# Performance work log

Hardware: AMD Instinct MI355X
Metric: run time of the kernel (lower is better)

## Reference

```python
import jax, jax.numpy as jnp
import numpy as np

N_NODES = 100000
N_EDGES = 1600000
D_IN = 128
D_HID = 128
SCALE = 1.8
EPS = 1e-12


def setup_inputs() -> dict:
    key = jax.random.key(0)
    ks = jax.random.split(key, 7)
    x = jax.random.normal(ks[0], (N_NODES, D_IN), dtype=jnp.float32)
    W1 = jax.random.normal(ks[1], (D_HID, D_IN), dtype=jnp.float32) * 0.05
    b1 = jax.random.normal(ks[2], (D_HID,), dtype=jnp.float32) * 0.05
    W2 = jax.random.normal(ks[3], (D_HID, D_HID), dtype=jnp.float32) * 0.05
    b2 = jax.random.normal(ks[4], (D_HID,), dtype=jnp.float32) * 0.05
    src = jax.random.randint(ks[5], (N_EDGES,), 0, N_NODES, dtype=jnp.int64 if jax.config.jax_enable_x64 else jnp.int32)
    dst = jax.random.randint(ks[6], (N_EDGES,), 0, N_NODES, dtype=jnp.int64 if jax.config.jax_enable_x64 else jnp.int32)
    return {"x": x, "W1": W1, "b1": b1, "W2": W2, "b2": b2, "src": src, "dst": dst}


def reference(x, W1, b1, W2, b2, src, dst):
    N = x.shape[0]
    ones = jnp.ones((src.shape[0],), dtype=x.dtype)
    # GraphConv norm='both' degree normalizers (clamped to >=1 as in DGL)
    deg_out = jnp.maximum(jnp.zeros((N,), x.dtype).at[src].add(ones), 1.0)
    deg_in = jnp.maximum(jnp.zeros((N,), x.dtype).at[dst].add(ones), 1.0)
    norm_out = jax.lax.rsqrt(deg_out)[:, None]  # [N,1]
    norm_in = jax.lax.rsqrt(deg_in)[:, None]    # [N,1]

    def layer(h, W, b):
        # torch.nn.Linear: h @ W.T + b
        h = jnp.einsum('nd,kd->nk', h, W) + b
        # F.normalize(h, dim=1) * 1.8
        nrm = jnp.sqrt(jnp.sum(h * h, axis=1, keepdims=True))
        h = h / jnp.maximum(nrm, EPS) * SCALE
        # GraphConv (weight=False, bias=False, norm='both'):
        # D_out^{-1/2} -> sparse aggregate -> D_in^{-1/2}
        h = h * norm_out
        agg = jax.ops.segment_sum(h[src], dst, num_segments=N)
        return agg * norm_in

    h = layer(x, W1, b1)
    h = layer(h, W2, b2)
    return h
```

## Files before the change

### kernel.cpp

```cpp
#include <hip/hip_runtime.h>
#include <cstdint>
#include <cstddef>

#define D 128
#define NSCALE 1.8f
#define NEPS 1e-12f
#define EPB 8192
#define NLO 512

typedef __attribute__((ext_vector_type(8))) short bf16x8;
typedef __attribute__((ext_vector_type(4))) float f32x4;

__device__ __forceinline__ ushort bf16_rtn(float f) {
    uint32_t u = __float_as_uint(f);
    u = u + 0x7FFFu + ((u >> 16) & 1u);
    return (ushort)(u >> 16);
}

__device__ __forceinline__ float bf16_to_f(ushort u) {
    return __uint_as_float((uint32_t)u << 16);
}

__global__ __launch_bounds__(256) void hist_high_kernel(const int* __restrict__ src,
                                                        const int* __restrict__ dst,
                                                        int* __restrict__ Hd,
                                                        int* __restrict__ Hs, int ne) {
    __shared__ int hd[256], hs[256];
    int t = threadIdx.x, b = blockIdx.x;
    hd[t] = 0; hs[t] = 0;
    __syncthreads();
    int base = b * EPB, end = min(ne, base + EPB);
    for (int i = base + t; i < end; i += 256) {
        atomicAdd(&hd[dst[i] >> 9], 1);
        atomicAdd(&hs[src[i] >> 9], 1);
    }
    __syncthreads();
    Hd[b * 256 + t] = hd[t];
    Hs[b * 256 + t] = hs[t];
}

__global__ __launch_bounds__(256) void scan_cols_kernel(int* __restrict__ Hd,
                                                        int* __restrict__ Hs,
                                                        int* __restrict__ total_d,
                                                        int* __restrict__ total_s, int nbk) {
    __shared__ int s[256];
    int* H = blockIdx.y ? Hs : Hd;
    int* tot = blockIdx.y ? total_s : total_d;
    int v = blockIdx.x, t = threadIdx.x;
    int val = (t < nbk) ? H[t * 256 + v] : 0;
    s[t] = val;
    __syncthreads();
    #pragma unroll
    for (int off = 1; off < 256; off <<= 1) {
        int u = (t >= off) ? s[t - off] : 0;
        __syncthreads();
        s[t] += u;
        __syncthreads();
    }
    if (t < nbk) H[t * 256 + v] = s[t] - val;
    if (t == nbk - 1) tot[v] = s[t];
}

__global__ __launch_bounds__(256) void scan_tot_kernel(const int* __restrict__ total_d,
                                                       const int* __restrict__ total_s,
                                                       int* __restrict__ Bd,
                                                       int* __restrict__ Bs, int hb) {
    __shared__ int s[256];
    const int* tot = blockIdx.x ? total_s : total_d;
    int* B = blockIdx.x ? Bs : Bd;
    int t = threadIdx.x;
    int val = (t < hb) ? tot[t] : 0;
    s[t] = val;
    __syncthreads();
    #pragma unroll
    for (int off = 1; off < 256; off <<= 1) {
        int u = (t >= off) ? s[t - off] : 0;
        __syncthreads();
        s[t] += u;
        __syncthreads();
    }
    if (t <= hb) B[t] = s[t] - val;
}

__global__ __launch_bounds__(256) void scatter_high_kernel(const int* __restrict__ src,
                                                           const int* __restrict__ dst,
                                                           const int* __restrict__ Hd,
                                                           const int* __restrict__ Hs,
                                                           const int* __restrict__ Bd,
                                                           const int* __restrict__ Bs,
                                                           int* __restrict__ sd_dst,
                                                           int* __restrict__ sd_src,
                                                           int* __restrict__ ss_src,
                                                           int ne, int hb) {
    __shared__ int cur_d[256], cur_s[256];
    int t = threadIdx.x, b = blockIdx.x;
    if (t < hb) {
        cur_d[t] = Bd[t] + Hd[b * 256 + t];
        cur_s[t] = Bs[t] + Hs[b * 256 + t];
    }
    __syncthreads();
    int base = b * EPB, end = min(ne, base + EPB);
    for (int i = base + t; i < end; i += 256) {
        int d = dst[i], s = src[i];
        int pd = atomicAdd(&cur_d[d >> 9], 1);
        sd_dst[pd] = d;
        sd_src[pd] = s;
        int ps = atomicAdd(&cur_s[s >> 9], 1);
        ss_src[ps] = s;
    }
}

__global__ __launch_bounds__(512) void bucket_sort_kernel(const int* __restrict__ sd_dst,
                                                          const int* __restrict__ sd_src,
                                                          const int* __restrict__ Bd,
                                                          int* __restrict__ offs,
                                                          int* __restrict__ cnt_dst,
                                                          float* __restrict__ norm_in,
                                                          int* __restrict__ ssrc, int N) {
    __shared__ int h[NLO], sc[NLO], cur[NLO];
    int t = threadIdx.x, v = blockIdx.x;
    int beg = Bd[v], end = Bd[v + 1];
    h[t] = 0;
    __syncthreads();
    for (int i = beg + t; i < end; i += 512) atomicAdd(&h[sd_dst[i] & (NLO - 1)], 1);
    __syncthreads();
    int cnt = h[t];
    sc[t] = cnt;
    __syncthreads();
    #pragma unroll
    for (int off = 1; off < NLO; off <<= 1) {
        int u = (t >= off) ? sc[t - off] : 0;
        __syncthreads();
        sc[t] += u;
        __syncthreads();
    }
    int excl = sc[t] - cnt;
    int g = (v << 9) + t;
    if (g < N) {
        offs[g] = beg + excl;
        cnt_dst[g] = cnt;
        norm_in[g] = rsqrtf((float)max(cnt, 1));
    }
    cur[t] = beg + excl;
    __syncthreads();
    for (int i = beg + t; i < end; i += 512) {
        int d = sd_dst[i];
        int s = sd_src[i];
        int p = atomicAdd(&cur[d & (NLO - 1)], 1);
        ssrc[p] = s;
    }
}

__global__ __launch_bounds__(512) void bucket_hist_kernel(const int* __restrict__ ss_src,
                                                          const int* __restrict__ Bs,
                                                          float* __restrict__ norm_out, int N) {
    __shared__ int h[NLO];
    int t = threadIdx.x, v = blockIdx.x;
    int beg = Bs[v], end = Bs[v + 1];
    h[t] = 0;
    __syncthreads();
    for (int i = beg + t; i < end; i += 512) atomicAdd(&h[ss_src[i] & (NLO - 1)], 1);
    __syncthreads();
    int g = (v << 9) + t;
    if (g < N) norm_out[g] = rsqrtf((float)max(h[t], 1));
}

__global__ __launch_bounds__(256) void mlp_mfma_kernel(const float* __restrict__ X,
                                                       const float* __restrict__ W,
                                                       const float* __restrict__ b,
                                                       const float* __restrict__ post,
                                                       ushort* __restrict__ Abuf, int N) {
    __shared__ ushort Wf[128 * 128];

    const int t = threadIdx.x;
    const int wave = t >> 6;
    const int lane = t & 63;
    const int q = lane >> 4;
    const int l16 = lane & 15;

    #pragma unroll
    for (int it = 0; it < 8; ++it) {
        int f = t + 256 * it;
        int j = f >> 8;
        int p = (f >> 6) & 3;
        int ln = f & 63;
        int n = 16 * j + (ln & 15);
        int k0 = 32 * p + 8 * (ln >> 4);
        const float* srcp = W + n * D + k0;
        float4 a0 = *(const float4*)(srcp);
        float4 a1 = *(const float4*)(srcp + 4);
        bf16x8 v;
        v[0] = (short)bf16_rtn(a0.x); v[1] = (short)bf16_rtn(a0.y);
        v[2] = (short)bf16_rtn(a0.z); v[3] = (short)bf16_rtn(a0.w);
        v[4] = (short)bf16_rtn(a1.x); v[5] = (short)bf16_rtn(a1.y);
        v[6] = (short)bf16_rtn(a1.z); v[7] = (short)bf16_rtn(a1.w);
        ((bf16x8*)Wf)[f] = v;
    }

    const int r0 = blockIdx.x * 128 + wave * 32;
    bf16x8 ahi[2][4], alo[2][4];
    #pragma unroll
    for (int rt = 0; rt < 2; ++rt) {
        int row = r0 + rt * 16 + l16;
        bool ok = (row < N);
        const float* xr = X + (size_t)(ok ? row : 0) * D;
        #pragma unroll
        for (int p = 0; p < 4; ++p) {
            int k0 = 32 * p + 8 * q;
            float4 a0 = ok ? *(const float4*)(xr + k0)     : make_float4(0, 0, 0, 0);
            float4 a1 = ok ? *(const float4*)(xr + k0 + 4) : make_float4(0, 0, 0, 0);
            float fv[8] = {a0.x, a0.y, a0.z, a0.w, a1.x, a1.y, a1.z, a1.w};
            bf16x8 h, l;
            #pragma unroll
            for (int e = 0; e < 8; ++e) {
                uint32_t u = __float_as_uint(fv[e]);
                h[e] = (short)(u >> 16);
                float hf = __uint_as_float(u & 0xFFFF0000u);
                l[e] = (short)(__float_as_uint(fv[e] - hf) >> 16);
            }
            ahi[rt][p] = h;
            alo[rt][p] = l;
        }
    }

    __syncthreads();

    f32x4 acc[2][8];
    #pragma unroll
    for (int rt = 0; rt < 2; ++rt)
        #pragma unroll
        for (int j = 0; j < 8; ++j) acc[rt][j] = (f32x4){0.f, 0.f, 0.f, 0.f};

    #pragma unroll
    for (int j = 0; j < 8; ++j) {
        #pragma unroll
        for (int p = 0; p < 4; ++p) {
            bf16x8 bb = ((bf16x8*)Wf)[(j * 4 + p) * 64 + lane];
            acc[0][j] = __builtin_amdgcn_mfma_f32_16x16x32_bf16(ahi[0][p], bb, acc[0][j], 0, 0, 0);
            acc[0][j] = __builtin_amdgcn_mfma_f32_16x16x32_bf16(alo[0][p], bb, acc[0][j], 0, 0, 0);
            acc[1][j] = __builtin_amdgcn_mfma_f32_16x16x32_bf16(ahi[1][p], bb, acc[1][j], 0, 0, 0);
            acc[1][j] = __builtin_amdgcn_mfma_f32_16x16x32_bf16(alo[1][p], bb, acc[1][j], 0, 0, 0);
        }
    }

    float bias[8];
    #pragma unroll
    for (int j = 0; j < 8; ++j) bias[j] = b[16 * j + l16];

    #pragma unroll
    for (int rt = 0; rt < 2; ++rt) {
        float ss[4] = {0.f, 0.f, 0.f, 0.f};
        #pragma unroll
        for (int j = 0; j < 8; ++j)
            #pragma unroll
            for (int r = 0; r < 4; ++r) {
                float v = acc[rt][j][r] + bias[j];
                acc[rt][j][r] = v;
                ss[r] += v * v;
            }
        #pragma unroll
        for (int m = 1; m <= 8; m <<= 1)
            #pragma unroll
            for (int r = 0; r < 4; ++r) ss[r] += __shfl_xor(ss[r], m);

        #pragma unroll
        for (int r = 0; r < 4; ++r) {
            int row = r0 + rt * 16 + 4 * q + r;
            if (row < N) {
                float f = NSCALE / fmaxf(sqrtf(ss[r]), NEPS) * post[row];
                #pragma unroll
                for (int j = 0; j < 8; ++j)
                    Abuf[(size_t)row * D + 16 * j + l16] = bf16_rtn(acc[rt][j][r] * f);
            }
        }
    }
}

__global__ __launch_bounds__(256) void agg_kernel(const ushort* __restrict__ A,
                                                  const int* __restrict__ sorted_src,
                                                  const int* __restrict__ offs,
                                                  const int* __restrict__ cnt,
                                                  const float* __restrict__ norm_in,
                                                  float* __restrict__ out, int N) {
    int g = (blockIdx.x * blockDim.x + threadIdx.x) >> 5;
    int lane = threadIdx.x & 31;
    if (g >= N) return;
    int beg = offs[g];
    int len = cnt[g];
    float4 acc = make_float4(0.f, 0.f, 0.f, 0.f);
    int i = 0;
    for (; i + 4 <= len; i += 4) {
        int s0 = sorted_src[beg + i];
        int s1 = sorted_src[beg + i + 1];
        int s2 = sorted_src[beg + i + 2];
        int s3 = sorted_src[beg + i + 3];
        ushort4 v0 = *(const ushort4*)(A + (size_t)s0 * D + lane * 4);
        ushort4 v1 = *(const ushort4*)(A + (size_t)s1 * D + lane * 4);
        ushort4 v2 = *(const ushort4*)(A + (size_t)s2 * D + lane * 4);
        ushort4 v3 = *(const ushort4*)(A + (size_t)s3 * D + lane * 4);
        acc.x += bf16_to_f(v0.x) + bf16_to_f(v1.x) + bf16_to_f(v2.x) + bf16_to_f(v3.x);
        acc.y += bf16_to_f(v0.y) + bf16_to_f(v1.y) + bf16_to_f(v2.y) + bf16_to_f(v3.y);
        acc.z += bf16_to_f(v0.z) + bf16_to_f(v1.z) + bf16_to_f(v2.z) + bf16_to_f(v3.z);
        acc.w += bf16_to_f(v0.w) + bf16_to_f(v1.w) + bf16_to_f(v2.w) + bf16_to_f(v3.w);
    }
    for (; i < len; ++i) {
        int s = sorted_src[beg + i];
        ushort4 v = *(const ushort4*)(A + (size_t)s * D + lane * 4);
        acc.x += bf16_to_f(v.x);
        acc.y += bf16_to_f(v.y);
        acc.z += bf16_to_f(v.z);
        acc.w += bf16_to_f(v.w);
    }
    float sc = norm_in[g];
    acc.x *= sc; acc.y *= sc; acc.z *= sc; acc.w *= sc;
    *(float4*)(out + (size_t)g * D + lane * 4) = acc;
}


extern "C" void kernel_launch(void* const* d_in, const int* in_sizes, int n_in,
                              void* d_out, int out_size, void* d_ws, size_t ws_size,
                              hipStream_t stream) {
    const float* x  = (const float*)d_in[0];
    const float* W1 = (const float*)d_in[1];
    const float* b1 = (const float*)d_in[2];
    const float* W2 = (const float*)d_in[3];
    const float* b2 = (const float*)d_in[4];
    const int* src  = (const int*)d_in[5];
    const int* dst  = (const int*)d_in[6];
    float* out = (float*)d_out;

    const int N  = in_sizes[0] / D;
    const int NE = in_sizes[5];
    const int NBK = (NE + EPB - 1) / EPB;
    const int HB  = (N + NLO - 1) / NLO;

    char* w = (char*)d_ws;
    auto take = [&](size_t bytes) { char* p = w; w += (bytes + 255) & ~(size_t)255; return p; };
    int*    Hd       = (int*)take((size_t)NBK * 256 * 4);
    int*    Hs       = (int*)take((size_t)NBK * 256 * 4);
    int*    total_d  = (int*)take(256 * 4);
    int*    total_s  = (int*)take(256 * 4);
    int*    Bd       = (int*)take((size_t)(HB + 1) * 4);
    int*    Bs       = (int*)take((size_t)(HB + 1) * 4);
    int*    sd_dst   = (int*)take((size_t)NE * 4);
    int*    sd_src   = (int*)take((size_t)NE * 4);
    int*    ss_src   = (int*)take((size_t)NE * 4);
    int*    ssrc     = (int*)take((size_t)NE * 4);
    int*    offs     = (int*)take((size_t)N * 4);
    int*    cnt_dst  = (int*)take((size_t)N * 4);
    float*  norm_in  = (float*)take((size_t)N * 4);
    float*  norm_out = (float*)take((size_t)N * 4);
    ushort* Abuf     = (ushort*)take((size_t)N * D * 2);

    hist_high_kernel<<<NBK, 256, 0, stream>>>(src, dst, Hd, Hs, NE);
    scan_cols_kernel<<<dim3(HB, 2), 256, 0, stream>>>(Hd, Hs, total_d, total_s, NBK);
    scan_tot_kernel<<<2, 256, 0, stream>>>(total_d, total_s, Bd, Bs, HB);
    scatter_high_kernel<<<NBK, 256, 0, stream>>>(src, dst, Hd, Hs, Bd, Bs,
                                                 sd_dst, sd_src, ss_src, NE, HB);
    bucket_sort_kernel<<<HB, 512, 0, stream>>>(sd_dst, sd_src, Bd, offs, cnt_dst,
                                               norm_in, ssrc, N);
    bucket_hist_kernel<<<HB, 512, 0, stream>>>(ss_src, Bs, norm_out, N);

    const int mlp_blocks = (N + 127) / 128;
    const int agg_blocks = (N * 32 + 255) / 256;

    mlp_mfma_kernel<<<mlp_blocks, 256, 0, stream>>>(x, W1, b1, norm_out, Abuf, N);
    agg_kernel<<<agg_blocks, 256, 0, stream>>>(Abuf, ssrc, offs, cnt_dst, norm_in, out, N);

    mlp_mfma_kernel<<<mlp_blocks, 256, 0, stream>>>(out, W2, b2, norm_out, Abuf, N);
    agg_kernel<<<agg_blocks, 256, 0, stream>>>(Abuf, ssrc, offs, cnt_dst, norm_in, out, N);
}
```

Baseline: 351.9 us.

## Restructure gather aggregation to 16B loads per lane and stage bucket sort in LDS

```diff
diff --git a/kernel.cpp b/kernel.cpp
--- a/kernel.cpp
+++ b/kernel.cpp
@@ -7,8 +7,10 @@
 #define NEPS 1e-12f
 #define EPB 8192
 #define NLO 512
+#define SCAP 9216
 
 typedef __attribute__((ext_vector_type(8))) short bf16x8;
+typedef __attribute__((ext_vector_type(8))) unsigned short u16x8;
 typedef __attribute__((ext_vector_type(4))) float f32x4;
 
 __device__ __forceinline__ ushort bf16_rtn(float f) {
@@ -88,8 +90,7 @@
                                                            const int* __restrict__ Hs,
                                                            const int* __restrict__ Bd,
                                                            const int* __restrict__ Bs,
-                                                           int* __restrict__ sd_dst,
-                                                           int* __restrict__ sd_src,
+                                                           int2* __restrict__ sd_pair,
                                                            int* __restrict__ ss_src,
                                                            int ne, int hb) {
     __shared__ int cur_d[256], cur_s[256];
@@ -103,26 +104,26 @@
     for (int i = base + t; i < end; i += 256) {
         int d = dst[i], s = src[i];
         int pd = atomicAdd(&cur_d[d >> 9], 1);
-        sd_dst[pd] = d;
-        sd_src[pd] = s;
+        sd_pair[pd] = make_int2(d, s);
         int ps = atomicAdd(&cur_s[s >> 9], 1);
         ss_src[ps] = s;
     }
 }
 
-__global__ __launch_bounds__(512) void bucket_sort_kernel(const int* __restrict__ sd_dst,
-                                                          const int* __restrict__ sd_src,
+__global__ __launch_bounds__(512) void bucket_sort_kernel(const int2* __restrict__ sd_pair,
                                                           const int* __restrict__ Bd,
                                                           int* __restrict__ offs,
                                                           int* __restrict__ cnt_dst,
                                                           float* __restrict__ norm_in,
                                                           int* __restrict__ ssrc, int N) {
     __shared__ int h[NLO], sc[NLO], cur[NLO];
+    __shared__ int stage[SCAP];
     int t = threadIdx.x, v = blockIdx.x;
     int beg = Bd[v], end = Bd[v + 1];
+    int m = end - beg;
     h[t] = 0;
     __syncthreads();
-    for (int i = beg + t; i < end; i += 512) atomicAdd(&h[sd_dst[i] & (NLO - 1)], 1);
+    for (int i = beg + t; i < end; i += 512) atomicAdd(&h[sd_pair[i].x & (NLO - 1)], 1);
     __syncthreads();
     int cnt = h[t];
     sc[t] = cnt;
@@ -141,13 +142,24 @@
         cnt_dst[g] = cnt;
         norm_in[g] = rsqrtf((float)max(cnt, 1));
     }
-    cur[t] = beg + excl;
-    __syncthreads();
-    for (int i = beg + t; i < end; i += 512) {
-        int d = sd_dst[i];
-        int s = sd_src[i];
-        int p = atomicAdd(&cur[d & (NLO - 1)], 1);
-        ssrc[p] = s;
+    if (m <= SCAP) {
+        cur[t] = excl;
+        __syncthreads();
+        for (int i = beg + t; i < end; i += 512) {
+            int2 p = sd_pair[i];
+            int pos = atomicAdd(&cur[p.x & (NLO - 1)], 1);
+            stage[pos] = p.y;
+        }
+        __syncthreads();
+        for (int j = t; j < m; j += 512) ssrc[beg + j] = stage[j];
+    } else {
+        cur[t] = beg + excl;
+        __syncthreads();
+        for (int i = beg + t; i < end; i += 512) {
+            int2 p = sd_pair[i];
+            int pos = atomicAdd(&cur[p.x & (NLO - 1)], 1);
+            ssrc[pos] = p.y;
+        }
     }
 }
 
@@ -282,38 +294,60 @@
                                                   const int* __restrict__ cnt,
                                                   const float* __restrict__ norm_in,
                                                   float* __restrict__ out, int N) {
-    int g = (blockIdx.x * blockDim.x + threadIdx.x) >> 5;
-    int lane = threadIdx.x & 31;
-    if (g >= N) return;
-    int beg = offs[g];
-    int len = cnt[g];
-    float4 acc = make_float4(0.f, 0.f, 0.f, 0.f);
+    int wave = threadIdx.x >> 6;
+    int node = blockIdx.x * 4 + wave;
+    if (node >= N) return;
+    int lane = threadIdx.x & 63;
+    int g = lane >> 4;
+    int c = lane & 15;
+    int beg = offs[node];
+    int len = cnt[node];
+    const ushort* Ac = A + c * 8;
+
+    float acc[8] = {0.f, 0.f, 0.f, 0.f, 0.f, 0.f, 0.f, 0.f};
     int i = 0;
+    for (; i + 16 <= len; i += 16) {
+        int s0 = sorted_src[beg + i + g];
+        int s1 = sorted_src[beg + i + 4 + g];
+        int s2 = sorted_src[beg + i + 8 + g];
+        int s3 = sorted_src[beg + i + 12 + g];
+        u16x8 v0 = *(const u16x8*)(Ac + (size_t)s0 * D);
+        u16x8 v1 = *(const u16x8*)(Ac + (size_t)s1 * D);
+        u16x8 v2 = *(const u16x8*)(Ac + (size_t)s2 * D);
+        u16x8 v3 = *(const u16x8*)(Ac + (size_t)s3 * D);
+        #pragma unroll
+        for (int e = 0; e < 8; ++e)
+            acc[e] += (bf16_to_f(v0[e]) + bf16_to_f(v1[e])) +
+                      (bf16_to_f(v2[e]) + bf16_to_f(v3[e]));
+    }
     for (; i + 4 <= len; i += 4) {
-        int s0 = sorted_src[beg + i];
-        int s1 = sorted_src[beg + i + 1];
-        int s2 = sorted_src[beg + i + 2];
-        int s3 = sorted_src[beg + i + 3];
-        ushort4 v0 = *(const ushort4*)(A + (size_t)s0 * D + lane * 4);
-        ushort4 v1 = *(const ushort4*)(A + (size_t)s1 * D + lane * 4);
-        ushort4 v2 = *(const ushort4*)(A + (size_t)s2 * D + lane * 4);
-        ushort4 v3 = *(const ushort4*)(A + (size_t)s3 * D + lane * 4);
-        acc.x += bf16_to_f(v0.x) + bf16_to_f(v1.x) + bf16_to_f(v2.x) + bf16_to_f(v3.x);
-        acc.y += bf16_to_f(v0.y) + bf16_to_f(v1.y) + bf16_to_f(v2.y) + bf16_to_f(v3.y);
-        acc.z += bf16_to_f(v0.z) + bf16_to_f(v1.z) + bf16_to_f(v2.z) + bf16_to_f(v3.z);
-        acc.w += bf16_to_f(v0.w) + bf16_to_f(v1.w) + bf16_to_f(v2.w) + bf16_to_f(v3.w);
-    }
-    for (; i < len; ++i) {
-        int s = sorted_src[beg + i];
-        ushort4 v = *(const ushort4*)(A + (size_t)s * D + lane * 4);
-        acc.x += bf16_to_f(v.x);
-        acc.y += bf16_to_f(v.y);
-        acc.z += bf16_to_f(v.z);
-        acc.w += bf16_to_f(v.w);
-    }
-    float sc = norm_in[g];
-    acc.x *= sc; acc.y *= sc; acc.z *= sc; acc.w *= sc;
-    *(float4*)(out + (size_t)g * D + lane * 4) = acc;
+        int s = sorted_src[beg + i + g];
+        u16x8 v = *(const u16x8*)(Ac + (size_t)s * D);
+        #pragma unroll
+        for (int e = 0; e < 8; ++e) acc[e] += bf16_to_f(v[e]);
+    }
+    int rem = len - i;
+    if (g < rem) {
+        int s = sorted_src[beg + i + g];
+        u16x8 v = *(const u16x8*)(Ac + (size_t)s * D);
+        #pragma unroll
+        for (int e = 0; e < 8; ++e) acc[e] += bf16_to_f(v[e]);
+    }
+
+    #pragma unroll
+    for (int e = 0; e < 8; ++e) {
+        acc[e] += __shfl_xor(acc[e], 16);
+        acc[e] += __shfl_xor(acc[e], 32);
+    }
+
+    if (g == 0) {
+        float sc = norm_in[node];
+        float4 w0 = make_float4(acc[0] * sc, acc[1] * sc, acc[2] * sc, acc[3] * sc);
+        float4 w1 = make_float4(acc[4] * sc, acc[5] * sc, acc[6] * sc, acc[7] * sc);
+        float* op = out + (size_t)node * D + c * 8;
+        *(float4*)(op) = w0;
+        *(float4*)(op + 4) = w1;
+    }
 }
 
 
@@ -342,8 +376,7 @@
     int*    total_s  = (int*)take(256 * 4);
     int*    Bd       = (int*)take((size_t)(HB + 1) * 4);
     int*    Bs       = (int*)take((size_t)(HB + 1) * 4);
-    int*    sd_dst   = (int*)take((size_t)NE * 4);
-    int*    sd_src   = (int*)take((size_t)NE * 4);
+    int2*   sd_pair  = (int2*)take((size_t)NE * 8);
     int*    ss_src   = (int*)take((size_t)NE * 4);
     int*    ssrc     = (int*)take((size_t)NE * 4);
     int*    offs     = (int*)take((size_t)N * 4);
@@ -356,13 +389,13 @@
     scan_cols_kernel<<<dim3(HB, 2), 256, 0, stream>>>(Hd, Hs, total_d, total_s, NBK);
     scan_tot_kernel<<<2, 256, 0, stream>>>(total_d, total_s, Bd, Bs, HB);
     scatter_high_kernel<<<NBK, 256, 0, stream>>>(src, dst, Hd, Hs, Bd, Bs,
-                                                 sd_dst, sd_src, ss_src, NE, HB);
-    bucket_sort_kernel<<<HB, 512, 0, stream>>>(sd_dst, sd_src, Bd, offs, cnt_dst,
+                                                 sd_pair, ss_src, NE, HB);
+    bucket_sort_kernel<<<HB, 512, 0, stream>>>(sd_pair, Bd, offs, cnt_dst,
                                                norm_in, ssrc, N);
     bucket_hist_kernel<<<HB, 512, 0, stream>>>(ss_src, Bs, norm_out, N);
 
     const int mlp_blocks = (N + 127) / 128;
-    const int agg_blocks = (N * 32 + 255) / 256;
+    const int agg_blocks = (N + 3) / 4;
 
     mlp_mfma_kernel<<<mlp_blocks, 256, 0, stream>>>(x, W1, b1, norm_out, Abuf, N);
     agg_kernel<<<agg_blocks, 256, 0, stream>>>(Abuf, ssrc, offs, cnt_dst, norm_in, out, N);
```

After: 341.8 us. 1.03x faster.
